# Optimization experiments

Hardware: AMD Instinct MI355X
Metric: run time of the kernel (lower is better)

## Reference

```python
import jax, jax.numpy as jnp
import numpy as np

N_NODES = 50000
N_EDGES = 1600000
D_FEAT = 32


def setup_inputs() -> dict:
    key = jax.random.key(0)
    k1, k2, k3, k4 = jax.random.split(key, 4)
    node_feat = jax.random.normal(k1, (N_NODES, D_FEAT), dtype=jnp.float32)
    edge_feat = jax.random.normal(k2, (N_EDGES, D_FEAT), dtype=jnp.float32)
    eps = jnp.zeros((1,), dtype=jnp.float32)  # learnable eps, init 0
    src = jax.random.randint(k3, (N_EDGES,), 0, N_NODES, dtype=jnp.int64)
    dst = jax.random.randint(k4, (N_EDGES,), 0, N_NODES, dtype=jnp.int64)
    return {"node_feat": node_feat, "edge_feat": edge_feat, "eps": eps,
            "src": src, "dst": dst}


def reference(node_feat, edge_feat, eps, src, dst):
    # message: relu(h_src + h_edge) per edge  [E, D]
    m = jax.nn.relu(node_feat[src] + edge_feat)
    # sum-aggregate messages into destination nodes  [N, D]
    neigh = jax.ops.segment_sum(m, dst, num_segments=node_feat.shape[0])
    # eps-scaled residual
    return (1.0 + eps[0]) * node_feat + neigh
```

## Files before the change

### kernel.cpp

```cpp
#include <hip/hip_runtime.h>

#define N_NODES 50000
#define N_EDGES 1600000
#define D_FEAT 32
#define SCAN_BLOCK 1024
#define N_SCAN_BLOCKS ((N_NODES + SCAN_BLOCK - 1) / SCAN_BLOCK)

#define WS_CNT   0
#define WS_EXCL  (N_NODES)
#define WS_OFF   (2 * N_NODES)
#define WS_BSUM  (3 * N_NODES)
#define WS_BSUMX (3 * N_NODES + 64)
#define WS_RANK  (3 * N_NODES + 128)
#define WS_MSG   (3 * N_NODES + 128 + N_EDGES)


__global__ void hist_rank(const int* __restrict__ dst,
                          int* __restrict__ cnt,
                          int* __restrict__ rank) {
    int e = blockIdx.x * blockDim.x + threadIdx.x;
    if (e < N_EDGES) rank[e] = atomicAdd(&cnt[dst[e]], 1);
}

__global__ void scan_blocks(const int* __restrict__ cnt,
                            int* __restrict__ excl,
                            int* __restrict__ bsum) {
    __shared__ int lds[SCAN_BLOCK];
    int tid = threadIdx.x;
    int i = blockIdx.x * SCAN_BLOCK + tid;
    int v = (i < N_NODES) ? cnt[i] : 0;
    int sum = v;
    lds[tid] = v;
    __syncthreads();
    for (int ofs = 1; ofs < SCAN_BLOCK; ofs <<= 1) {
        int t = (tid >= ofs) ? lds[tid - ofs] : 0;
        __syncthreads();
        sum += t;
        lds[tid] = sum;
        __syncthreads();
    }
    if (i < N_NODES) excl[i] = sum - v;
    if (tid == SCAN_BLOCK - 1) bsum[blockIdx.x] = lds[SCAN_BLOCK - 1];
}

__global__ void scan_bsums(const int* __restrict__ bsum, int* __restrict__ bsumx) {
    int lane = threadIdx.x;
    int orig = (lane < N_SCAN_BLOCKS) ? bsum[lane] : 0;
    int v = orig;
    for (int o = 1; o < 64; o <<= 1) {
        int t = __shfl_up(v, o);
        if (lane >= o) v += t;
    }
    if (lane < N_SCAN_BLOCKS) bsumx[lane] = v - orig;
}

__global__ void finalize_off(const int* __restrict__ excl,
                             const int* __restrict__ bsumx,
                             int* __restrict__ off) {
    int i = blockIdx.x * SCAN_BLOCK + threadIdx.x;
    if (i < N_NODES) off[i] = excl[i] + bsumx[blockIdx.x];
}

__global__ void build_msg(const float* __restrict__ node_feat,
                          const float* __restrict__ edge_feat,
                          const int* __restrict__ src,
                          const int* __restrict__ dst,
                          const int* __restrict__ off,
                          const int* __restrict__ rank,
                          float* __restrict__ msg) {
    int t = blockIdx.x * blockDim.x + threadIdx.x;
    int e = t >> 3;
    int g = t & 7;
    if (e >= N_EDGES) return;

    int d = dst[e];
    int pos = off[d] + rank[e];
    int s = src[e];

    float4 ef = ((const float4*)edge_feat)[(size_t)e * 8 + g];
    float4 nf = ((const float4*)node_feat)[s * 8 + g];
    float4 m;
    m.x = fmaxf(nf.x + ef.x, 0.f);
    m.y = fmaxf(nf.y + ef.y, 0.f);
    m.z = fmaxf(nf.z + ef.z, 0.f);
    m.w = fmaxf(nf.w + ef.w, 0.f);
    ((float4*)msg)[(size_t)pos * 8 + g] = m;
}

__global__ void reduce_msgs(const float* __restrict__ node_feat,
                            const float* __restrict__ eps,
                            const int* __restrict__ off,
                            const int* __restrict__ cnt,
                            const float* __restrict__ msg,
                            float* __restrict__ out) {
    int t = blockIdx.x * blockDim.x + threadIdx.x;
    int n = t >> 3;
    int g = t & 7;
    if (n >= N_NODES) return;

    int start = off[n];
    int c = cnt[n];

    float4 acc = make_float4(0.f, 0.f, 0.f, 0.f);
    for (int i = 0; i < c; ++i) {
        float4 m = ((const float4*)msg)[(size_t)(start + i) * 8 + g];
        acc.x += m.x; acc.y += m.y; acc.z += m.z; acc.w += m.w;
    }

    float scale = 1.0f + eps[0];
    float4 h = ((const float4*)node_feat)[n * 8 + g];
    float4 o;
    o.x = scale * h.x + acc.x;
    o.y = scale * h.y + acc.y;
    o.z = scale * h.z + acc.z;
    o.w = scale * h.w + acc.w;
    ((float4*)out)[n * 8 + g] = o;
}


__global__ void fb_init_out(const float* __restrict__ node_feat,
                            const float* __restrict__ eps,
                            float* __restrict__ out) {
    int i = blockIdx.x * blockDim.x + threadIdx.x;
    const int n4 = N_NODES * D_FEAT / 4;
    float scale = 1.0f + eps[0];
    if (i < n4) {
        float4 v = ((const float4*)node_feat)[i];
        v.x *= scale; v.y *= scale; v.z *= scale; v.w *= scale;
        ((float4*)out)[i] = v;
    }
}

__global__ void fb_scatter(const float* __restrict__ node_feat,
                           const float* __restrict__ edge_feat,
                           const int* __restrict__ src,
                           const int* __restrict__ dst,
                           float* __restrict__ out) {
    int t = blockIdx.x * blockDim.x + threadIdx.x;
    int e = t >> 3;
    int g = t & 7;
    if (e >= N_EDGES) return;
    int s = src[e];
    int d = dst[e];
    float4 nf = ((const float4*)node_feat)[s * 8 + g];
    float4 ef = ((const float4*)edge_feat)[(size_t)e * 8 + g];
    float* op = out + (size_t)d * D_FEAT + g * 4;
    unsafeAtomicAdd(op + 0, fmaxf(nf.x + ef.x, 0.f));
    unsafeAtomicAdd(op + 1, fmaxf(nf.y + ef.y, 0.f));
    unsafeAtomicAdd(op + 2, fmaxf(nf.z + ef.z, 0.f));
    unsafeAtomicAdd(op + 3, fmaxf(nf.w + ef.w, 0.f));
}

extern "C" void kernel_launch(void* const* d_in, const int* in_sizes, int n_in,
                              void* d_out, int out_size, void* d_ws, size_t ws_size,
                              hipStream_t stream) {
    const float* node_feat = (const float*)d_in[0];
    const float* edge_feat = (const float*)d_in[1];
    const float* eps       = (const float*)d_in[2];
    const int*   src       = (const int*)d_in[3];
    const int*   dst       = (const int*)d_in[4];
    float* out = (float*)d_out;

    const int B = 256;
    const size_t need = ((size_t)WS_MSG + (size_t)N_EDGES * D_FEAT) * sizeof(int);

    if (ws_size < need) {
        int n4 = N_NODES * D_FEAT / 4;
        fb_init_out<<<(n4 + B - 1) / B, B, 0, stream>>>(node_feat, eps, out);
        long long total = (long long)N_EDGES * 8;
        fb_scatter<<<(int)((total + B - 1) / B), B, 0, stream>>>(
            node_feat, edge_feat, src, dst, out);
        return;
    }

    int* ws = (int*)d_ws;
    int*   cnt   = ws + WS_CNT;
    int*   excl  = ws + WS_EXCL;
    int*   off   = ws + WS_OFF;
    int*   bsum  = ws + WS_BSUM;
    int*   bsumx = ws + WS_BSUMX;
    int*   rank  = ws + WS_RANK;
    float* msg   = (float*)(ws + WS_MSG);

    hipMemsetAsync(cnt, 0, N_NODES * sizeof(int), stream);

    hist_rank<<<(N_EDGES + B - 1) / B, B, 0, stream>>>(dst, cnt, rank);
    scan_blocks<<<N_SCAN_BLOCKS, SCAN_BLOCK, 0, stream>>>(cnt, excl, bsum);
    scan_bsums<<<1, 64, 0, stream>>>(bsum, bsumx);
    finalize_off<<<N_SCAN_BLOCKS, SCAN_BLOCK, 0, stream>>>(excl, bsumx, off);

    long long etotal = (long long)N_EDGES * 8;
    build_msg<<<(int)((etotal + B - 1) / B), B, 0, stream>>>(
        node_feat, edge_feat, src, dst, off, rank, msg);

    long long ntotal = (long long)N_NODES * 8;
    reduce_msgs<<<(int)((ntotal + B - 1) / B), B, 0, stream>>>(
        node_feat, eps, off, cnt, msg, out);
}
```

Before: 511.3 us.

## Sort edge index pairs instead of materializing messages, gather features in reduce

Instead of writing a full 1.6M×32 float message buffer in CSR order and reading it back, the code now scatters only (edge id, src id) pairs into dst-sorted order. The reduce kernel loads eight pairs per group, broadcasts them with shuffles, and gathers edge and node features directly, computing relu(sum) on the fly. The finalize_off kernel is folded into the consumers, which now compute the offset from excl plus bsumx. This removes about 400 MB of message write and read traffic. In exchange, the edge_feat reads become random gathers, and this relies on nontemporal loads to limit cache pollution.

```diff
diff --git a/kernel.cpp b/kernel.cpp
--- a/kernel.cpp
+++ b/kernel.cpp
@@ -8,11 +8,12 @@
 
 #define WS_CNT   0
 #define WS_EXCL  (N_NODES)
-#define WS_OFF   (2 * N_NODES)
-#define WS_BSUM  (3 * N_NODES)
-#define WS_BSUMX (3 * N_NODES + 64)
-#define WS_RANK  (3 * N_NODES + 128)
-#define WS_MSG   (3 * N_NODES + 128 + N_EDGES)
+#define WS_BSUM  (2 * N_NODES)
+#define WS_BSUMX (2 * N_NODES + 64)
+#define WS_RANK  (2 * N_NODES + 128)
+#define WS_PAIR  (2 * N_NODES + 128 + N_EDGES)
+
+typedef float f4 __attribute__((ext_vector_type(4)));
 
 
 __global__ void hist_rank(const int* __restrict__ dst,
@@ -54,67 +55,78 @@
     if (lane < N_SCAN_BLOCKS) bsumx[lane] = v - orig;
 }
 
-__global__ void finalize_off(const int* __restrict__ excl,
-                             const int* __restrict__ bsumx,
-                             int* __restrict__ off) {
-    int i = blockIdx.x * SCAN_BLOCK + threadIdx.x;
-    if (i < N_NODES) off[i] = excl[i] + bsumx[blockIdx.x];
-}
-
-__global__ void build_msg(const float* __restrict__ node_feat,
-                          const float* __restrict__ edge_feat,
-                          const int* __restrict__ src,
-                          const int* __restrict__ dst,
-                          const int* __restrict__ off,
-                          const int* __restrict__ rank,
-                          float* __restrict__ msg) {
-    int t = blockIdx.x * blockDim.x + threadIdx.x;
-    int e = t >> 3;
-    int g = t & 7;
+__global__ void scatter_pairs(const int* __restrict__ src,
+                              const int* __restrict__ dst,
+                              const int* __restrict__ excl,
+                              const int* __restrict__ bsumx,
+                              const int* __restrict__ rank,
+                              int2* __restrict__ pair) {
+    int e = blockIdx.x * blockDim.x + threadIdx.x;
     if (e >= N_EDGES) return;
-
     int d = dst[e];
-    int pos = off[d] + rank[e];
-    int s = src[e];
-
-    float4 ef = ((const float4*)edge_feat)[(size_t)e * 8 + g];
-    float4 nf = ((const float4*)node_feat)[s * 8 + g];
-    float4 m;
-    m.x = fmaxf(nf.x + ef.x, 0.f);
-    m.y = fmaxf(nf.y + ef.y, 0.f);
-    m.z = fmaxf(nf.z + ef.z, 0.f);
-    m.w = fmaxf(nf.w + ef.w, 0.f);
-    ((float4*)msg)[(size_t)pos * 8 + g] = m;
-}
-
-__global__ void reduce_msgs(const float* __restrict__ node_feat,
-                            const float* __restrict__ eps,
-                            const int* __restrict__ off,
-                            const int* __restrict__ cnt,
-                            const float* __restrict__ msg,
-                            float* __restrict__ out) {
+    int pos = excl[d] + bsumx[d >> 10] + rank[e];
+    pair[pos] = make_int2(e, src[e]);
+}
+
+__global__ void reduce_gather(const float* __restrict__ node_feat,
+                              const float* __restrict__ edge_feat,
+                              const float* __restrict__ eps,
+                              const int* __restrict__ excl,
+                              const int* __restrict__ bsumx,
+                              const int* __restrict__ cnt,
+                              const int2* __restrict__ pair,
+                              float* __restrict__ out) {
     int t = blockIdx.x * blockDim.x + threadIdx.x;
     int n = t >> 3;
     int g = t & 7;
     if (n >= N_NODES) return;
 
-    int start = off[n];
+    int start = excl[n] + bsumx[n >> 10];
     int c = cnt[n];
-
-    float4 acc = make_float4(0.f, 0.f, 0.f, 0.f);
-    for (int i = 0; i < c; ++i) {
-        float4 m = ((const float4*)msg)[(size_t)(start + i) * 8 + g];
-        acc.x += m.x; acc.y += m.y; acc.z += m.z; acc.w += m.w;
+    int gbase = (threadIdx.x & 63) & ~7;
+
+    const f4* efp = (const f4*)edge_feat;
+    const f4* nfp = (const f4*)node_feat;
+
+    f4 acc = (f4)(0.f);
+    int i0 = 0;
+    for (; i0 + 8 <= c; i0 += 8) {
+        int2 p = pair[start + i0 + g];
+#pragma unroll
+        for (int j = 0; j < 8; ++j) {
+            int e = __shfl(p.x, gbase + j);
+            int s = __shfl(p.y, gbase + j);
+            f4 ef = __builtin_nontemporal_load(&efp[(size_t)e * 8 + g]);
+            f4 nf = nfp[(size_t)s * 8 + g];
+            acc.x += fmaxf(nf.x + ef.x, 0.f);
+            acc.y += fmaxf(nf.y + ef.y, 0.f);
+            acc.z += fmaxf(nf.z + ef.z, 0.f);
+            acc.w += fmaxf(nf.w + ef.w, 0.f);
+        }
+    }
+    int rem = c - i0;
+    if (rem > 0) {
+        int2 p = (g < rem) ? pair[start + i0 + g] : make_int2(0, 0);
+        for (int j = 0; j < rem; ++j) {
+            int e = __shfl(p.x, gbase + j);
+            int s = __shfl(p.y, gbase + j);
+            f4 ef = __builtin_nontemporal_load(&efp[(size_t)e * 8 + g]);
+            f4 nf = nfp[(size_t)s * 8 + g];
+            acc.x += fmaxf(nf.x + ef.x, 0.f);
+            acc.y += fmaxf(nf.y + ef.y, 0.f);
+            acc.z += fmaxf(nf.z + ef.z, 0.f);
+            acc.w += fmaxf(nf.w + ef.w, 0.f);
+        }
     }
 
     float scale = 1.0f + eps[0];
-    float4 h = ((const float4*)node_feat)[n * 8 + g];
-    float4 o;
+    f4 h = nfp[(size_t)n * 8 + g];
+    f4 o;
     o.x = scale * h.x + acc.x;
     o.y = scale * h.y + acc.y;
     o.z = scale * h.z + acc.z;
     o.w = scale * h.w + acc.w;
-    ((float4*)out)[n * 8 + g] = o;
+    ((f4*)out)[(size_t)n * 8 + g] = o;
 }
 
 
@@ -162,7 +174,7 @@
     float* out = (float*)d_out;
 
     const int B = 256;
-    const size_t need = ((size_t)WS_MSG + (size_t)N_EDGES * D_FEAT) * sizeof(int);
+    const size_t need = ((size_t)WS_PAIR + 2ull * N_EDGES) * sizeof(int);
 
     if (ws_size < need) {
         int n4 = N_NODES * D_FEAT / 4;
@@ -174,26 +186,23 @@
     }
 
     int* ws = (int*)d_ws;
-    int*   cnt   = ws + WS_CNT;
-    int*   excl  = ws + WS_EXCL;
-    int*   off   = ws + WS_OFF;
-    int*   bsum  = ws + WS_BSUM;
-    int*   bsumx = ws + WS_BSUMX;
-    int*   rank  = ws + WS_RANK;
-    float* msg   = (float*)(ws + WS_MSG);
+    int*  cnt   = ws + WS_CNT;
+    int*  excl  = ws + WS_EXCL;
+    int*  bsum  = ws + WS_BSUM;
+    int*  bsumx = ws + WS_BSUMX;
+    int*  rank  = ws + WS_RANK;
+    int2* pair  = (int2*)(ws + WS_PAIR);
 
     hipMemsetAsync(cnt, 0, N_NODES * sizeof(int), stream);
 
     hist_rank<<<(N_EDGES + B - 1) / B, B, 0, stream>>>(dst, cnt, rank);
     scan_blocks<<<N_SCAN_BLOCKS, SCAN_BLOCK, 0, stream>>>(cnt, excl, bsum);
     scan_bsums<<<1, 64, 0, stream>>>(bsum, bsumx);
-    finalize_off<<<N_SCAN_BLOCKS, SCAN_BLOCK, 0, stream>>>(excl, bsumx, off);
-
-    long long etotal = (long long)N_EDGES * 8;
-    build_msg<<<(int)((etotal + B - 1) / B), B, 0, stream>>>(
-        node_feat, edge_feat, src, dst, off, rank, msg);
+
+    scatter_pairs<<<(N_EDGES + B - 1) / B, B, 0, stream>>>(
+        src, dst, excl, bsumx, rank, pair);
 
     long long ntotal = (long long)N_NODES * 8;
-    reduce_msgs<<<(int)((ntotal + B - 1) / B), B, 0, stream>>>(
-        node_feat, eps, off, cnt, msg, out);
-}
+    reduce_gather<<<(int)((ntotal + B - 1) / B), B, 0, stream>>>(
+        node_feat, edge_feat, eps, excl, bsumx, cnt, pair, out);
+}
```

After: 434.7 us. -15.0%, faster.

## Replace counting-sort gather with direct float atomic scatter into output

Applied to the files above, without the earlier changes.

Drops the histogram, scan, message buffer build and segmented reduction pipeline. Output is now initialised to the scaled node features and each edge's relu message is added straight into its destination row with unsafe float atomics. This removes six launches, the 200 MB message buffer write and its re-read. In exchange it relies on atomic throughput under destination contention and makes the summation order nondeterministic.

```diff
diff --git a/kernel.cpp b/kernel.cpp
--- a/kernel.cpp
+++ b/kernel.cpp
@@ -3,152 +3,43 @@
 #define N_NODES 50000
 #define N_EDGES 1600000
 #define D_FEAT 32
-#define SCAN_BLOCK 1024
-#define N_SCAN_BLOCKS ((N_NODES + SCAN_BLOCK - 1) / SCAN_BLOCK)
 
-#define WS_CNT   0
-#define WS_EXCL  (N_NODES)
-#define WS_OFF   (2 * N_NODES)
-#define WS_BSUM  (3 * N_NODES)
-#define WS_BSUMX (3 * N_NODES + 64)
-#define WS_RANK  (3 * N_NODES + 128)
-#define WS_MSG   (3 * N_NODES + 128 + N_EDGES)
+typedef float f4 __attribute__((ext_vector_type(4)));
 
-
-__global__ void hist_rank(const int* __restrict__ dst,
-                          int* __restrict__ cnt,
-                          int* __restrict__ rank) {
-    int e = blockIdx.x * blockDim.x + threadIdx.x;
-    if (e < N_EDGES) rank[e] = atomicAdd(&cnt[dst[e]], 1);
-}
-
-__global__ void scan_blocks(const int* __restrict__ cnt,
-                            int* __restrict__ excl,
-                            int* __restrict__ bsum) {
-    __shared__ int lds[SCAN_BLOCK];
-    int tid = threadIdx.x;
-    int i = blockIdx.x * SCAN_BLOCK + tid;
-    int v = (i < N_NODES) ? cnt[i] : 0;
-    int sum = v;
-    lds[tid] = v;
-    __syncthreads();
-    for (int ofs = 1; ofs < SCAN_BLOCK; ofs <<= 1) {
-        int t = (tid >= ofs) ? lds[tid - ofs] : 0;
-        __syncthreads();
-        sum += t;
-        lds[tid] = sum;
-        __syncthreads();
-    }
-    if (i < N_NODES) excl[i] = sum - v;
-    if (tid == SCAN_BLOCK - 1) bsum[blockIdx.x] = lds[SCAN_BLOCK - 1];
-}
-
-__global__ void scan_bsums(const int* __restrict__ bsum, int* __restrict__ bsumx) {
-    int lane = threadIdx.x;
-    int orig = (lane < N_SCAN_BLOCKS) ? bsum[lane] : 0;
-    int v = orig;
-    for (int o = 1; o < 64; o <<= 1) {
-        int t = __shfl_up(v, o);
-        if (lane >= o) v += t;
-    }
-    if (lane < N_SCAN_BLOCKS) bsumx[lane] = v - orig;
-}
-
-__global__ void finalize_off(const int* __restrict__ excl,
-                             const int* __restrict__ bsumx,
-                             int* __restrict__ off) {
-    int i = blockIdx.x * SCAN_BLOCK + threadIdx.x;
-    if (i < N_NODES) off[i] = excl[i] + bsumx[blockIdx.x];
-}
-
-__global__ void build_msg(const float* __restrict__ node_feat,
-                          const float* __restrict__ edge_feat,
-                          const int* __restrict__ src,
-                          const int* __restrict__ dst,
-                          const int* __restrict__ off,
-                          const int* __restrict__ rank,
-                          float* __restrict__ msg) {
-    int t = blockIdx.x * blockDim.x + threadIdx.x;
-    int e = t >> 3;
-    int g = t & 7;
-    if (e >= N_EDGES) return;
-
-    int d = dst[e];
-    int pos = off[d] + rank[e];
-    int s = src[e];
-
-    float4 ef = ((const float4*)edge_feat)[(size_t)e * 8 + g];
-    float4 nf = ((const float4*)node_feat)[s * 8 + g];
-    float4 m;
-    m.x = fmaxf(nf.x + ef.x, 0.f);
-    m.y = fmaxf(nf.y + ef.y, 0.f);
-    m.z = fmaxf(nf.z + ef.z, 0.f);
-    m.w = fmaxf(nf.w + ef.w, 0.f);
-    ((float4*)msg)[(size_t)pos * 8 + g] = m;
-}
-
-__global__ void reduce_msgs(const float* __restrict__ node_feat,
-                            const float* __restrict__ eps,
-                            const int* __restrict__ off,
-                            const int* __restrict__ cnt,
-                            const float* __restrict__ msg,
-                            float* __restrict__ out) {
-    int t = blockIdx.x * blockDim.x + threadIdx.x;
-    int n = t >> 3;
-    int g = t & 7;
-    if (n >= N_NODES) return;
-
-    int start = off[n];
-    int c = cnt[n];
-
-    float4 acc = make_float4(0.f, 0.f, 0.f, 0.f);
-    for (int i = 0; i < c; ++i) {
-        float4 m = ((const float4*)msg)[(size_t)(start + i) * 8 + g];
-        acc.x += m.x; acc.y += m.y; acc.z += m.z; acc.w += m.w;
-    }
-
-    float scale = 1.0f + eps[0];
-    float4 h = ((const float4*)node_feat)[n * 8 + g];
-    float4 o;
-    o.x = scale * h.x + acc.x;
-    o.y = scale * h.y + acc.y;
-    o.z = scale * h.z + acc.z;
-    o.w = scale * h.w + acc.w;
-    ((float4*)out)[n * 8 + g] = o;
-}
-
-
-__global__ void fb_init_out(const float* __restrict__ node_feat,
-                            const float* __restrict__ eps,
-                            float* __restrict__ out) {
+__global__ void init_out(const float* __restrict__ node_feat,
+                         const float* __restrict__ eps,
+                         float* __restrict__ out) {
     int i = blockIdx.x * blockDim.x + threadIdx.x;
     const int n4 = N_NODES * D_FEAT / 4;
     float scale = 1.0f + eps[0];
     if (i < n4) {
-        float4 v = ((const float4*)node_feat)[i];
-        v.x *= scale; v.y *= scale; v.z *= scale; v.w *= scale;
-        ((float4*)out)[i] = v;
+        f4 v = ((const f4*)node_feat)[i];
+        ((f4*)out)[i] = v * scale;
     }
 }
 
-__global__ void fb_scatter(const float* __restrict__ node_feat,
-                           const float* __restrict__ edge_feat,
-                           const int* __restrict__ src,
-                           const int* __restrict__ dst,
-                           float* __restrict__ out) {
+__global__ void fuse_scatter(const float* __restrict__ node_feat,
+                             const float* __restrict__ edge_feat,
+                             const int* __restrict__ src,
+                             const int* __restrict__ dst,
+                             float* __restrict__ out) {
     int t = blockIdx.x * blockDim.x + threadIdx.x;
     int e = t >> 3;
     int g = t & 7;
     if (e >= N_EDGES) return;
     int s = src[e];
     int d = dst[e];
-    float4 nf = ((const float4*)node_feat)[s * 8 + g];
-    float4 ef = ((const float4*)edge_feat)[(size_t)e * 8 + g];
+    f4 ef = ((const f4*)edge_feat)[(size_t)e * 8 + g];
+    f4 nf = ((const f4*)node_feat)[(size_t)s * 8 + g];
+    float m0 = fmaxf(nf.x + ef.x, 0.f);
+    float m1 = fmaxf(nf.y + ef.y, 0.f);
+    float m2 = fmaxf(nf.z + ef.z, 0.f);
+    float m3 = fmaxf(nf.w + ef.w, 0.f);
     float* op = out + (size_t)d * D_FEAT + g * 4;
-    unsafeAtomicAdd(op + 0, fmaxf(nf.x + ef.x, 0.f));
-    unsafeAtomicAdd(op + 1, fmaxf(nf.y + ef.y, 0.f));
-    unsafeAtomicAdd(op + 2, fmaxf(nf.z + ef.z, 0.f));
-    unsafeAtomicAdd(op + 3, fmaxf(nf.w + ef.w, 0.f));
+    unsafeAtomicAdd(op + 0, m0);
+    unsafeAtomicAdd(op + 1, m1);
+    unsafeAtomicAdd(op + 2, m2);
+    unsafeAtomicAdd(op + 3, m3);
 }
 
 extern "C" void kernel_launch(void* const* d_in, const int* in_sizes, int n_in,
@@ -162,38 +53,11 @@
     float* out = (float*)d_out;
 
     const int B = 256;
-    const size_t need = ((size_t)WS_MSG + (size_t)N_EDGES * D_FEAT) * sizeof(int);
 
-    if (ws_size < need) {
-        int n4 = N_NODES * D_FEAT / 4;
-        fb_init_out<<<(n4 + B - 1) / B, B, 0, stream>>>(node_feat, eps, out);
-        long long total = (long long)N_EDGES * 8;
-        fb_scatter<<<(int)((total + B - 1) / B), B, 0, stream>>>(
-            node_feat, edge_feat, src, dst, out);
-        return;
-    }
+    int n4 = N_NODES * D_FEAT / 4;
+    init_out<<<(n4 + B - 1) / B, B, 0, stream>>>(node_feat, eps, out);
 
-    int* ws = (int*)d_ws;
-    int*   cnt   = ws + WS_CNT;
-    int*   excl  = ws + WS_EXCL;
-    int*   off   = ws + WS_OFF;
-    int*   bsum  = ws + WS_BSUM;
-    int*   bsumx = ws + WS_BSUMX;
-    int*   rank  = ws + WS_RANK;
-    float* msg   = (float*)(ws + WS_MSG);
-
-    hipMemsetAsync(cnt, 0, N_NODES * sizeof(int), stream);
-
-    hist_rank<<<(N_EDGES + B - 1) / B, B, 0, stream>>>(dst, cnt, rank);
-    scan_blocks<<<N_SCAN_BLOCKS, SCAN_BLOCK, 0, stream>>>(cnt, excl, bsum);
-    scan_bsums<<<1, 64, 0, stream>>>(bsum, bsumx);
-    finalize_off<<<N_SCAN_BLOCKS, SCAN_BLOCK, 0, stream>>>(excl, bsumx, off);
-
-    long long etotal = (long long)N_EDGES * 8;
-    build_msg<<<(int)((etotal + B - 1) / B), B, 0, stream>>>(
-        node_feat, edge_feat, src, dst, off, rank, msg);
-
-    long long ntotal = (long long)N_NODES * 8;
-    reduce_msgs<<<(int)((ntotal + B - 1) / B), B, 0, stream>>>(
-        node_feat, eps, off, cnt, msg, out);
+    long long total = (long long)N_EDGES * 8;
+    fuse_scatter<<<(int)((total + B - 1) / B), B, 0, stream>>>(
+        node_feat, edge_feat, src, dst, out);
 }
```

Result: slower. 869.0 us (+69.9%).
